# Kernel optimization log

Measured on AMD Instinct MI355X. Metric: run time of the kernel, lower is better.

## Reference

```python
import jax, jax.numpy as jnp
import numpy as np

D_MODEL = 1024
NUM_HEADS = 16
HEAD_DIM = D_MODEL // NUM_HEADS


def setup_inputs() -> dict:
    key = jax.random.key(0)
    k1, k2, k3, k4, k5 = jax.random.split(key, 5)
    scale = 1.0 / np.sqrt(D_MODEL)
    x = jax.random.normal(k1, (8, 1024, D_MODEL), dtype=jnp.float32)
    # weights stored (in, out) so y = x @ W + b (same math as torch Linear)
    Wqkv = jax.random.normal(k2, (D_MODEL, 3 * D_MODEL), dtype=jnp.float32) * scale
    bqkv = jax.random.normal(k3, (3 * D_MODEL,), dtype=jnp.float32) * scale
    Wo = jax.random.normal(k4, (D_MODEL, D_MODEL), dtype=jnp.float32) * scale
    bo = jax.random.normal(k5, (D_MODEL,), dtype=jnp.float32) * scale
    return {"x": x, "Wqkv": Wqkv, "bqkv": bqkv, "Wo": Wo, "bo": bo}


def reference(x, Wqkv, bqkv, Wo, bo):
    B, S, D = x.shape
    H, Hd = NUM_HEADS, HEAD_DIM
    # fused QKV projection: [B,S,3D]
    qkv = jnp.einsum('bsd,de->bse', x, Wqkv) + bqkv
    # reshape -> [B,S,H,3*Hd] -> [B,H,S,3*Hd], then chunk
    qkv = qkv.reshape(B, S, H, 3 * Hd).transpose(0, 2, 1, 3)
    q, k, v = jnp.split(qkv, 3, axis=-1)  # each [B,H,S,Hd]
    scores = jnp.einsum('bhqd,bhkd->bhqk', q, k) / jnp.sqrt(jnp.asarray(Hd, x.dtype))
    attn = jax.nn.softmax(scores, axis=-1)
    vals = jnp.einsum('bhqk,bhkd->bhqd', attn, v)  # [B,H,S,Hd]
    vals = vals.transpose(0, 2, 1, 3).reshape(B, S, D)
    out = jnp.einsum('bsd,de->bse', vals, Wo) + bo
    return out
```

## Files before the change

### kernel.cpp

```cpp
#include <hip/hip_runtime.h>
#include <hip/hip_bf16.h>
#include <stdint.h>


typedef __bf16 bf16;
typedef __bf16 bf16x8 __attribute__((ext_vector_type(8)));
typedef float f32x4 __attribute__((ext_vector_type(4)));

__device__ __forceinline__ void async_copy16(const bf16* g, bf16* l) {
  void* gv = (void*)g;
  __builtin_amdgcn_global_load_lds((__attribute__((address_space(1))) void*)gv,
                                   (__attribute__((address_space(3))) void*)l,
                                   16, 0, 0);
}

__global__ __launch_bounds__(256) void convert_kernel(const float* __restrict__ in,
                                                      bf16* __restrict__ out, int n) {
  int i = (blockIdx.x * 256 + threadIdx.x) * 8;
  if (i >= n) return;
  float4 a = *(const float4*)(in + i);
  float4 b = *(const float4*)(in + i + 4);
  bf16x8 v;
  v[0] = (bf16)a.x; v[1] = (bf16)a.y; v[2] = (bf16)a.z; v[3] = (bf16)a.w;
  v[4] = (bf16)b.x; v[5] = (bf16)b.y; v[6] = (bf16)b.z; v[7] = (bf16)b.w;
  *(bf16x8*)(out + i) = v;
}

__global__ __launch_bounds__(256) void wt_kernel(const float* __restrict__ in,
                                                 bf16* __restrict__ out,
                                                 int R, int C) {
  __shared__ bf16 tile[64][65];
  const int c0 = blockIdx.x * 64;
  const int r0 = blockIdx.y * 64;
  const int tid = threadIdx.x;
  const int c = tid & 63, g = tid >> 6;
#pragma unroll
  for (int j = 0; j < 16; j++) {
    int r = j * 4 + g;
    tile[r][c] = (bf16)in[(size_t)(r0 + r) * C + c0 + c];
  }
  __syncthreads();
#pragma unroll
  for (int j = 0; j < 16; j++) {
    int r = j * 4 + g;
    out[(size_t)(c0 + r) * R + r0 + c] = tile[c][r];
  }
}

__global__ __launch_bounds__(256) void vt_kernel(const bf16* __restrict__ qkv,
                                                 bf16* __restrict__ Vt) {
  __shared__ bf16 tile[64][65];
  const int tid = threadIdx.x;
  const int s0 = blockIdx.x * 64;
  const int bh = blockIdx.y;
  const int b = bh >> 4, h = bh & 15;
  const int c = tid & 63, g = tid >> 6;
  const bf16* src = qkv + ((size_t)b * 1024 + s0) * 3072 + h * 192 + 128;
#pragma unroll
  for (int j = 0; j < 16; j++) {
    int s = j * 4 + g;
    tile[s][c] = src[(size_t)s * 3072 + c];
  }
  __syncthreads();
  bf16* dst = Vt + (size_t)bh * 64 * 1024 + s0;
#pragma unroll
  for (int j = 0; j < 16; j++) {
    int d = j * 4 + g;
    dst[(size_t)d * 1024 + c] = tile[c][d];
  }
}

template <typename OutT>
__global__ __launch_bounds__(256, 2)
void gemm_bt_bias(const bf16* __restrict__ A, const bf16* __restrict__ Bt,
                  const float* __restrict__ bias, OutT* __restrict__ C,
                  int N, int K) {
  __shared__ __align__(16) bf16 As[128 * 64];
  __shared__ __align__(16) bf16 Bs[128 * 64];
  const int tid = threadIdx.x;
  const int lane = tid & 63;
  const int w = tid >> 6;
  const int m0 = blockIdx.y * 128;
  const int n0 = blockIdx.x * 128;
  const int wm = (w & 1) * 64;
  const int wn = (w >> 1) * 64;
  const int l15 = lane & 15, g8 = lane >> 4, l7 = lane & 7;

  f32x4 acc[4][4] = {};

  const int sr = tid >> 3;
  const int scs = ((tid & 7) ^ (sr & 7)) * 8;
  const bf16* Ag = A + (size_t)(m0 + sr) * K + scs;
  const bf16* Bg = Bt + (size_t)(n0 + sr) * K + scs;

  for (int k0 = 0; k0 < K; k0 += 64) {
    __syncthreads();
#pragma unroll
    for (int m = 0; m < 4; m++) {
      async_copy16(Ag + (size_t)(32 * m) * K + k0, &As[m * 2048 + tid * 8]);
      async_copy16(Bg + (size_t)(32 * m) * K + k0, &Bs[m * 2048 + tid * 8]);
    }
    __syncthreads();
#pragma unroll
    for (int ks = 0; ks < 2; ks++) {
      const int ch = ((ks * 4 + g8) ^ l7) * 8;
      bf16x8 af[4], bfr[4];
#pragma unroll
      for (int mt = 0; mt < 4; mt++)
        af[mt] = *(const bf16x8*)&As[(wm + mt * 16 + l15) * 64 + ch];
#pragma unroll
      for (int nt = 0; nt < 4; nt++)
        bfr[nt] = *(const bf16x8*)&Bs[(wn + nt * 16 + l15) * 64 + ch];
#pragma unroll
      for (int mt = 0; mt < 4; mt++)
#pragma unroll
        for (int nt = 0; nt < 4; nt++)
          acc[mt][nt] = __builtin_amdgcn_mfma_f32_16x16x32_bf16(af[mt], bfr[nt], acc[mt][nt], 0, 0, 0);
    }
  }

  const int rowg = g8 * 4;
#pragma unroll
  for (int nt = 0; nt < 4; nt++) {
    int n = n0 + wn + nt * 16 + l15;
    float bv = bias[n];
#pragma unroll
    for (int mt = 0; mt < 4; mt++) {
      int mbase = m0 + wm + mt * 16 + rowg;
#pragma unroll
      for (int r = 0; r < 4; r++)
        C[(size_t)(mbase + r) * N + n] = (OutT)(acc[mt][nt][r] + bv);
    }
  }
}

#define PS_STRIDE 72
__global__ __launch_bounds__(256, 4)
void attn_kernel(const bf16* __restrict__ qkv, const bf16* __restrict__ Vt,
                 bf16* __restrict__ vals) {
  __shared__ __align__(16) bf16 smem[64 * 64 * 2 + 128 * PS_STRIDE];
  bf16* const Qs = smem;
  bf16* const Ks = smem;
  bf16* const Vs = smem + 4096;
  bf16* const Ps = smem + 8192;
  const int tid = threadIdx.x;
  const int lane = tid & 63;
  const int w = tid >> 6;
  const int bh = blockIdx.x;
  const int q0 = blockIdx.y * 128;
  const int b = bh >> 4, h = bh & 15;
  const size_t tok0 = (size_t)b * 1024;
  const int l15 = lane & 15, g8 = lane >> 4, l7 = lane & 7;

  {
    const int r = tid >> 3;
    const int cs = ((tid & 7) ^ (r & 7)) * 8;
    const bf16* g = qkv + (tok0 + q0 + r) * 3072 + h * 192 + cs;
    async_copy16(g, &Qs[tid * 8]);
    async_copy16(g + (size_t)32 * 3072, &Qs[2048 + tid * 8]);
    async_copy16(g + (size_t)64 * 3072, &Qs[4096 + tid * 8]);
    async_copy16(g + (size_t)96 * 3072, &Qs[6144 + tid * 8]);
  }
  __syncthreads();

  bf16x8 aq[2][2];
#pragma unroll
  for (int ks = 0; ks < 2; ks++) {
    const int ch = ((ks * 4 + g8) ^ l7) * 8;
#pragma unroll
    for (int mt = 0; mt < 2; mt++)
      aq[mt][ks] = *(const bf16x8*)&Qs[(w * 32 + mt * 16 + l15) * 64 + ch];
  }
  __builtin_amdgcn_s_waitcnt(0xC07F);

  f32x4 O[2][4] = {};
  f32x4 lacc[2] = {};
  bf16x8 ones;
#pragma unroll
  for (int j = 0; j < 8; j++) ones[j] = (bf16)1.0f;

  const int kr = tid >> 3;
  const int kcs = ((tid & 7) ^ (kr & 7)) * 8;
  const float scale = 0.125f;

  for (int kt = 0; kt < 16; kt++) {
    const int k0 = kt * 64;
    __syncthreads();
    {
      const bf16* kg = qkv + (tok0 + k0 + kr) * 3072 + h * 192 + 64 + kcs;
      async_copy16(kg, &Ks[tid * 8]);
      async_copy16(kg + (size_t)32 * 3072, &Ks[2048 + tid * 8]);
      const bf16* vg = Vt + ((size_t)bh * 64 + kr) * 1024 + k0 + kcs;
      async_copy16(vg, &Vs[tid * 8]);
      async_copy16(vg + (size_t)32 * 1024, &Vs[2048 + tid * 8]);
    }
    __syncthreads();

    f32x4 S[2][4] = {};
#pragma unroll
    for (int ks = 0; ks < 2; ks++) {
      const int ch = ((ks * 4 + g8) ^ l7) * 8;
      bf16x8 bfr[4];
#pragma unroll
      for (int nt = 0; nt < 4; nt++)
        bfr[nt] = *(const bf16x8*)&Ks[(nt * 16 + l15) * 64 + ch];
#pragma unroll
      for (int mt = 0; mt < 2; mt++)
#pragma unroll
        for (int nt = 0; nt < 4; nt++)
          S[mt][nt] = __builtin_amdgcn_mfma_f32_16x16x32_bf16(aq[mt][ks], bfr[nt], S[mt][nt], 0, 0, 0);
    }

#pragma unroll
    for (int mt = 0; mt < 2; mt++) {
#pragma unroll
      for (int nt = 0; nt < 4; nt++) {
        int q = w * 32 + mt * 16 + g8 * 4;
        int c = nt * 16 + l15;
#pragma unroll
        for (int r = 0; r < 4; r++)
          Ps[(q + r) * PS_STRIDE + c] = (bf16)__expf(S[mt][nt][r] * scale);
      }
    }

#pragma unroll
    for (int ks = 0; ks < 2; ks++) {
      const int ch = ((ks * 4 + g8) ^ l7) * 8;
      bf16x8 af[2], bfr[4];
#pragma unroll
      for (int mt = 0; mt < 2; mt++)
        af[mt] = *(const bf16x8*)&Ps[(w * 32 + mt * 16 + l15) * PS_STRIDE + ks * 32 + g8 * 8];
#pragma unroll
      for (int dt = 0; dt < 4; dt++)
        bfr[dt] = *(const bf16x8*)&Vs[(dt * 16 + l15) * 64 + ch];
#pragma unroll
      for (int mt = 0; mt < 2; mt++) {
#pragma unroll
        for (int dt = 0; dt < 4; dt++)
          O[mt][dt] = __builtin_amdgcn_mfma_f32_16x16x32_bf16(af[mt], bfr[dt], O[mt][dt], 0, 0, 0);
        lacc[mt] = __builtin_amdgcn_mfma_f32_16x16x32_bf16(af[mt], ones, lacc[mt], 0, 0, 0);
      }
    }
  }

#pragma unroll
  for (int mt = 0; mt < 2; mt++) {
    int qb = q0 + w * 32 + mt * 16 + g8 * 4;
    f32x4 rinv;
#pragma unroll
    for (int r = 0; r < 4; r++) rinv[r] = 1.0f / lacc[mt][r];
#pragma unroll
    for (int dt = 0; dt < 4; dt++) {
      int d = h * 64 + dt * 16 + l15;
#pragma unroll
      for (int r = 0; r < 4; r++)
        vals[(tok0 + qb + r) * 1024 + d] = (bf16)(O[mt][dt][r] * rinv[r]);
    }
  }
}

extern "C" void kernel_launch(void* const* d_in, const int* in_sizes, int n_in,
                              void* d_out, int out_size, void* d_ws, size_t ws_size,
                              hipStream_t stream) {
  const float* x    = (const float*)d_in[0];
  const float* Wqkv = (const float*)d_in[1];
  const float* bqkv = (const float*)d_in[2];
  const float* Wo   = (const float*)d_in[3];
  const float* bo   = (const float*)d_in[4];
  float* out = (float*)d_out;

  uint8_t* ws = (uint8_t*)d_ws;
  bf16* qkv  = (bf16*)(ws);
  bf16* Wqkt = (bf16*)(ws + 48u * 1024 * 1024);
  bf16* Wot  = (bf16*)(ws + 54u * 1024 * 1024);
  bf16* Vt   = (bf16*)(ws + 56u * 1024 * 1024);
  bf16* vals = (bf16*)(ws + 72u * 1024 * 1024);
  bf16* xb   = (bf16*)(ws + 88u * 1024 * 1024);

  const int nx = 8 * 1024 * 1024;
  convert_kernel<<<nx / (256 * 8), 256, 0, stream>>>(x, xb, nx);
  wt_kernel<<<dim3(48, 16), 256, 0, stream>>>(Wqkv, Wqkt, 1024, 3072);
  wt_kernel<<<dim3(16, 16), 256, 0, stream>>>(Wo, Wot, 1024, 1024);
  gemm_bt_bias<bf16><<<dim3(24, 64), 256, 0, stream>>>(xb, Wqkt, bqkv, qkv, 3072, 1024);
  vt_kernel<<<dim3(16, 128), 256, 0, stream>>>(qkv, Vt);
  attn_kernel<<<dim3(128, 8), 256, 0, stream>>>(qkv, Vt, vals);
  gemm_bt_bias<float><<<dim3(8, 64), 256, 0, stream>>>(vals, Wot, bo, out, 1024, 1024);
}
```

Measured before the change: 233.9 us.

## Merge prep kernels and fuse V transpose into QKV GEMM epilogue

Combines the x conversion and both weight transposes into one prep kernel, removing two launches. The QKV GEMM epilogue now writes the V columns directly in transposed layout, which drops the separate vt_kernel and its extra read and write pass over V. Softmax exponentials switch to exp2f with the log2(e) factor folded into the scale. The transposed V store scatters 4-element vectors with a 2KB stride, so it may coalesce poorly compared with the old row-major writes.

```diff
diff --git a/kernel.cpp b/kernel.cpp
--- a/kernel.cpp
+++ b/kernel.cpp
@@ -4,6 +4,7 @@
 
 
 typedef __bf16 bf16;
+typedef __bf16 bf16x4 __attribute__((ext_vector_type(4)));
 typedef __bf16 bf16x8 __attribute__((ext_vector_type(8)));
 typedef float f32x4 __attribute__((ext_vector_type(4)));
 
@@ -14,25 +15,11 @@
                                    16, 0, 0);
 }
 
-__global__ __launch_bounds__(256) void convert_kernel(const float* __restrict__ in,
-                                                      bf16* __restrict__ out, int n) {
-  int i = (blockIdx.x * 256 + threadIdx.x) * 8;
-  if (i >= n) return;
-  float4 a = *(const float4*)(in + i);
-  float4 b = *(const float4*)(in + i + 4);
-  bf16x8 v;
-  v[0] = (bf16)a.x; v[1] = (bf16)a.y; v[2] = (bf16)a.z; v[3] = (bf16)a.w;
-  v[4] = (bf16)b.x; v[5] = (bf16)b.y; v[6] = (bf16)b.z; v[7] = (bf16)b.w;
-  *(bf16x8*)(out + i) = v;
-}
-
-__global__ __launch_bounds__(256) void wt_kernel(const float* __restrict__ in,
-                                                 bf16* __restrict__ out,
-                                                 int R, int C) {
-  __shared__ bf16 tile[64][65];
-  const int c0 = blockIdx.x * 64;
-  const int r0 = blockIdx.y * 64;
-  const int tid = threadIdx.x;
+__device__ __forceinline__ void wt_body(const float* __restrict__ in,
+                                        bf16* __restrict__ out,
+                                        int R, int C, int bx, int by,
+                                        int tid, bf16 (*tile)[65]) {
+  const int c0 = bx * 64, r0 = by * 64;
   const int c = tid & 63, g = tid >> 6;
 #pragma unroll
   for (int j = 0; j < 16; j++) {
@@ -47,34 +34,37 @@
   }
 }
 
-__global__ __launch_bounds__(256) void vt_kernel(const bf16* __restrict__ qkv,
-                                                 bf16* __restrict__ Vt) {
+__global__ __launch_bounds__(256) void prep_kernel(const float* __restrict__ x,
+                                                   bf16* __restrict__ xb,
+                                                   const float* __restrict__ Wqkv,
+                                                   bf16* __restrict__ Wqkt,
+                                                   const float* __restrict__ Wo,
+                                                   bf16* __restrict__ Wot) {
   __shared__ bf16 tile[64][65];
+  const int bid = blockIdx.x;
   const int tid = threadIdx.x;
-  const int s0 = blockIdx.x * 64;
-  const int bh = blockIdx.y;
-  const int b = bh >> 4, h = bh & 15;
-  const int c = tid & 63, g = tid >> 6;
-  const bf16* src = qkv + ((size_t)b * 1024 + s0) * 3072 + h * 192 + 128;
-#pragma unroll
-  for (int j = 0; j < 16; j++) {
-    int s = j * 4 + g;
-    tile[s][c] = src[(size_t)s * 3072 + c];
-  }
-  __syncthreads();
-  bf16* dst = Vt + (size_t)bh * 64 * 1024 + s0;
-#pragma unroll
-  for (int j = 0; j < 16; j++) {
-    int d = j * 4 + g;
-    dst[(size_t)d * 1024 + c] = tile[c][d];
-  }
-}
-
-template <typename OutT>
+  if (bid < 4096) {
+    int i = (bid * 256 + tid) * 8;
+    float4 a = *(const float4*)(x + i);
+    float4 b = *(const float4*)(x + i + 4);
+    bf16x8 v;
+    v[0] = (bf16)a.x; v[1] = (bf16)a.y; v[2] = (bf16)a.z; v[3] = (bf16)a.w;
+    v[4] = (bf16)b.x; v[5] = (bf16)b.y; v[6] = (bf16)b.z; v[7] = (bf16)b.w;
+    *(bf16x8*)(xb + i) = v;
+  } else if (bid < 4096 + 768) {
+    int idx = bid - 4096;
+    wt_body(Wqkv, Wqkt, 1024, 3072, idx % 48, idx / 48, tid, tile);
+  } else {
+    int idx = bid - 4864;
+    wt_body(Wo, Wot, 1024, 1024, idx % 16, idx / 16, tid, tile);
+  }
+}
+
+template <typename OutT, bool WITH_VT>
 __global__ __launch_bounds__(256, 2)
 void gemm_bt_bias(const bf16* __restrict__ A, const bf16* __restrict__ Bt,
                   const float* __restrict__ bias, OutT* __restrict__ C,
-                  int N, int K) {
+                  bf16* __restrict__ Vt, int N, int K) {
   __shared__ __align__(16) bf16 As[128 * 64];
   __shared__ __align__(16) bf16 Bs[128 * 64];
   const int tid = threadIdx.x;
@@ -122,14 +112,24 @@
   const int rowg = g8 * 4;
 #pragma unroll
   for (int nt = 0; nt < 4; nt++) {
-    int n = n0 + wn + nt * 16 + l15;
-    float bv = bias[n];
+    const int n = n0 + wn + nt * 16 + l15;
+    const float bv = bias[n];
+    const bool vpart = WITH_VT && (((n >> 6) % 3) == 2);
 #pragma unroll
     for (int mt = 0; mt < 4; mt++) {
-      int mbase = m0 + wm + mt * 16 + rowg;
-#pragma unroll
-      for (int r = 0; r < 4; r++)
-        C[(size_t)(mbase + r) * N + n] = (OutT)(acc[mt][nt][r] + bv);
+      const int mbase = m0 + wm + mt * 16 + rowg;
+      if (vpart) {
+        const int h = n / 192, d = n & 63;
+        const int b = mbase >> 10, s = mbase & 1023;
+        bf16x4 v;
+#pragma unroll
+        for (int r = 0; r < 4; r++) v[r] = (bf16)(acc[mt][nt][r] + bv);
+        *(bf16x4*)&Vt[(((size_t)(b * 16 + h) * 64 + d) << 10) + s] = v;
+      } else {
+#pragma unroll
+        for (int r = 0; r < 4; r++)
+          C[(size_t)(mbase + r) * N + n] = (OutT)(acc[mt][nt][r] + bv);
+      }
     }
   }
 }
@@ -181,7 +181,7 @@
 
   const int kr = tid >> 3;
   const int kcs = ((tid & 7) ^ (kr & 7)) * 8;
-  const float scale = 0.125f;
+  const float c2 = 0.18033688f;
 
   for (int kt = 0; kt < 16; kt++) {
     const int k0 = kt * 64;
@@ -219,7 +219,7 @@
         int c = nt * 16 + l15;
 #pragma unroll
         for (int r = 0; r < 4; r++)
-          Ps[(q + r) * PS_STRIDE + c] = (bf16)__expf(S[mt][nt][r] * scale);
+          Ps[(q + r) * PS_STRIDE + c] = (bf16)exp2f(S[mt][nt][r] * c2);
       }
     }
 
@@ -277,12 +277,8 @@
   bf16* vals = (bf16*)(ws + 72u * 1024 * 1024);
   bf16* xb   = (bf16*)(ws + 88u * 1024 * 1024);
 
-  const int nx = 8 * 1024 * 1024;
-  convert_kernel<<<nx / (256 * 8), 256, 0, stream>>>(x, xb, nx);
-  wt_kernel<<<dim3(48, 16), 256, 0, stream>>>(Wqkv, Wqkt, 1024, 3072);
-  wt_kernel<<<dim3(16, 16), 256, 0, stream>>>(Wo, Wot, 1024, 1024);
-  gemm_bt_bias<bf16><<<dim3(24, 64), 256, 0, stream>>>(xb, Wqkt, bqkv, qkv, 3072, 1024);
-  vt_kernel<<<dim3(16, 128), 256, 0, stream>>>(qkv, Vt);
+  prep_kernel<<<5120, 256, 0, stream>>>(x, xb, Wqkv, Wqkt, Wo, Wot);
+  gemm_bt_bias<bf16, true><<<dim3(24, 64), 256, 0, stream>>>(xb, Wqkt, bqkv, qkv, Vt, 3072, 1024);
   attn_kernel<<<dim3(128, 8), 256, 0, stream>>>(qkv, Vt, vals);
-  gemm_bt_bias<float><<<dim3(8, 64), 256, 0, stream>>>(vals, Wot, bo, out, 1024, 1024);
-}
+  gemm_bt_bias<float, false><<<dim3(8, 64), 256, 0, stream>>>(vals, Wot, bo, out, nullptr, 1024, 1024);
+}
```

Measured after the change: 249.4 us. 6.6% more time.
